# Kernel tuning notes

Measured on AMD Instinct MI355X. Metric: run time of the kernel, lower is better.

The kernel has to match this reference:

```python
import jax, jax.numpy as jnp
import numpy as np

HID = 512
NHEADS = 8
HEAD_DIM = HID // NHEADS  # 64
L = 2048
B = 4
LQ = 128
SCALE = float(np.sqrt(HEAD_DIM))


def _xavier(k, shape):
    lim = float(np.sqrt(6.0 / (shape[0] + shape[1])))
    return jax.random.uniform(k, shape, jnp.float32, -lim, lim)


def setup_inputs() -> dict:
    key = jax.random.key(0)
    ks = jax.random.split(key, 9)
    query = jax.random.normal(ks[0], (L, B, HID), jnp.float32)
    key_t = jax.random.normal(ks[1], (L, B, HID), jnp.float32)
    value = jax.random.normal(ks[2], (L, B, HID), jnp.float32)
    # 1 = pad, 0 = valid (code adds (1-mask).log() to scores)
    key_padding_mask = jax.random.bernoulli(ks[3], 0.1, (B, L)).astype(jnp.float32)
    question_rel_emb = jax.random.normal(ks[4], (LQ, LQ, B, HID), jnp.float32) * 0.02
    Wq = _xavier(ks[5], (HID, HID))
    Wk = _xavier(ks[6], (HID, HID))
    Wv = _xavier(ks[7], (HID, HID))
    Wo = _xavier(ks[8], (HID, HID))
    return dict(query=query, key_t=key_t, value=value,
                key_padding_mask=key_padding_mask,
                question_rel_emb=question_rel_emb,
                Wq=Wq, Wk=Wk, Wv=Wv, Wo=Wo)


def reference(query, key_t, value, key_padding_mask, question_rel_emb, Wq, Wk, Wv, Wo):
    # head_reshape: [L,B,HID] -> [B*K, L, D] (b outer, k inner, matching torch view)
    def heads(x, W):
        y = x @ W.T                                   # [L,B,HID]
        return jnp.swapaxes(y.reshape(L, B * NHEADS, HEAD_DIM), 0, 1)

    q = heads(query, Wq)    # [BK,L,D]
    k = heads(key_t, Wk)
    v = heads(value, Wv)

    attn = jnp.einsum('nld,nmd->nlm', q, k)            # [BK,L,L]

    # question relative bias: proj_key over [Lq,Lq,B,HID] -> [BK,Lq,Lq,D]
    qr = question_rel_emb @ Wk.T
    qr = qr.reshape(LQ, LQ, B * NHEADS, HEAD_DIM).transpose(2, 0, 1, 3)
    bias = jnp.einsum('nijd,nid->nij', qr, q[:, -LQ:])  # [BK,Lq,Lq]
    attn = attn.at[:, -LQ:, -LQ:].add(bias)

    attn = attn / SCALE

    # padding mask: repeat_interleave over batch, add log(1-mask) per key column
    kpm = jnp.repeat(key_padding_mask, NHEADS, axis=0)  # [BK,L]
    attn = attn + jnp.log1p(-kpm)[:, None, :]

    attn = jax.nn.softmax(attn, axis=-1)
    out = jnp.einsum('nlm,nmd->nld', attn, v)           # [BK,L,D]
    out = jnp.swapaxes(out, 0, 1).reshape(L, B, HID) @ Wo.T
    return (out, attn)
```

## Files before the change

### kernel.cpp

```cpp
#include <hip/hip_runtime.h>
#include <hip/hip_bf16.h>


using short8   = __attribute__((ext_vector_type(8))) short;
using short4v  = __attribute__((ext_vector_type(4))) short;
using ushort4v = __attribute__((ext_vector_type(4))) unsigned short;
using f32x4    = __attribute__((ext_vector_type(4))) float;

#define L_T   2048
#define B_T   4
#define HID_T 512
#define HD_T  64
#define LQ_T  128
#define L0_T  1920

__device__ __forceinline__ float b2f(unsigned short u){
  return __uint_as_float(((unsigned int)u) << 16);
}
__device__ __forceinline__ unsigned short f2b(float f){
  unsigned int u = __float_as_uint(f);
  u += 0x7FFFu + ((u >> 16) & 1u);
  return (unsigned short)(u >> 16);
}
__device__ __forceinline__ f32x4 mfma16(short8 a, short8 b, f32x4 c){
  return __builtin_amdgcn_mfma_f32_16x16x32_bf16(a, b, c, 0, 0, 0);
}
#if __has_builtin(__builtin_amdgcn_mfma_f32_16x16x16bf16_1k)
__device__ __forceinline__ f32x4 mfma16k16(short4v a, short4v b, f32x4 c){
  return __builtin_amdgcn_mfma_f32_16x16x16bf16_1k(a, b, c, 0, 0, 0);
}
#else
__device__ __forceinline__ f32x4 mfma16k16(short4v a, short4v b, f32x4 c){
  f32x4 d;
  asm("v_mfma_f32_16x16x16_bf16 %0, %1, %2, %0"
      : "=v"(d) : "v"(a), "v"(b), "0"(c));
  return d;
}
#endif

__global__ __launch_bounds__(256) void k_splitW(const float* __restrict__ w0,
                                                const float* __restrict__ w1,
                                                const float* __restrict__ w2,
                                                const float* __restrict__ w3,
                                                unsigned short* __restrict__ hi,
                                                unsigned short* __restrict__ lo)
{
  int wid = blockIdx.y;
  const float* src = (wid == 0) ? w0 : (wid == 1) ? w1 : (wid == 2) ? w2 : w3;
  int chunk = blockIdx.x * 256 + threadIdx.x;
  int o = chunk >> 7;
  int hpos = (chunk & 127) * 4;
  f32x4 v = ((const f32x4*)src)[chunk];
  ushort4v h4, l4;
  #pragma unroll
  for (int e = 0; e < 4; e++){
    unsigned short h = f2b(v[e]);
    h4[e] = h;
    l4[e] = f2b(v[e] - b2f(h));
  }
  size_t idx = ((size_t)(wid * 512 + (o >> 4) * 16 + (hpos >> 5))) * 512
             + (((hpos & 31) >> 3) * 16 + (o & 15)) * 8 + (hpos & 7);
  *(ushort4v*)(hi + idx) = h4;
  *(ushort4v*)(lo + idx) = l4;
}

__global__ __launch_bounds__(256) void k_proj3(const float* __restrict__ Xq,
                                               const float* __restrict__ Xk,
                                               const float* __restrict__ Xv,
                                               const unsigned short* __restrict__ WhA,
                                               const unsigned short* __restrict__ WlA,
                                               unsigned short* __restrict__ qhp,
                                               unsigned short* __restrict__ qlp,
                                               unsigned short* __restrict__ khp,
                                               unsigned short* __restrict__ klp,
                                               unsigned short* __restrict__ vpk)
{
  int sel = blockIdx.x >> 10;
  int bx  = blockIdx.x & 1023;
  const float* X = (sel == 0) ? Xq : (sel == 1) ? Xk : Xv;
  const short* WH = (const short*)WhA + (size_t)sel * 262144;
  const short* WL = (const short*)WlA + (size_t)sel * 262144;
  unsigned short* ohi = (sel == 0) ? qhp : khp;
  unsigned short* olo = (sel == 0) ? qlp : klp;

  int wv = threadIdx.x >> 6, lane = threadIdx.x & 63;
  int tid = bx * 4 + wv;
  int mt = tid >> 3, nt = tid & 7;
  int row0 = mt * 16, col0 = nt * 64;
  int lhi = lane >> 4, llo = lane & 15;
  int arow = row0 + llo;
  f32x4 acc[4] = {{0,0,0,0},{0,0,0,0},{0,0,0,0},{0,0,0,0}};
  #pragma unroll 4
  for (int k0 = 0; k0 < 512; k0 += 32){
    const float* ap = X + (size_t)arow * 512 + k0 + lhi * 8;
    f32x4 a01 = *(const f32x4*)ap;
    f32x4 a23 = *(const f32x4*)(ap + 4);
    short8 ah, al;
    #pragma unroll
    for (int e = 0; e < 4; e++){
      unsigned short h0 = f2b(a01[e]);
      ah[e] = (short)h0;  al[e] = (short)f2b(a01[e] - b2f(h0));
      unsigned short h1 = f2b(a23[e]);
      ah[e + 4] = (short)h1;  al[e + 4] = (short)f2b(a23[e] - b2f(h1));
    }
    int kk = k0 >> 5;
    #pragma unroll
    for (int cb = 0; cb < 4; cb++){
      size_t bidx = (size_t)(((col0 >> 4) + cb) * 16 + kk) * 512 + lane * 8;
      short8 bh = *(const short8*)(WH + bidx);
      short8 bl = *(const short8*)(WL + bidx);
      acc[cb] = mfma16(ah, bh, acc[cb]);
      acc[cb] = mfma16(al, bh, acc[cb]);
      acc[cb] = mfma16(ah, bl, acc[cb]);
    }
  }
  #pragma unroll
  for (int cb = 0; cb < 4; cb++){
    #pragma unroll
    for (int r = 0; r < 4; r++){
      int row = row0 + lhi * 4 + r;
      int o   = col0 + cb * 16 + llo;
      int l = row >> 2, bb = row & 3;
      int n = bb * 8 + (o >> 6), d = o & 63;
      float v = acc[cb][r];
      if (sel != 2){
        size_t idx = ((size_t)(n * 128 + (l >> 4)) * 2 + (d >> 5)) * 512
                   + (((d & 31) >> 3) * 16 + (l & 15)) * 8 + (d & 7);
        unsigned short h = f2b(v);
        ohi[idx] = h;
        olo[idx] = f2b(v - b2f(h));
      } else {
        int m = l;
        size_t idx = (((size_t)(n * 128 + (m >> 4)) * 4) + (d >> 4)) * 256
                   + ((m & 15) >> 2) * 64 + (d & 15) * 4 + (m & 3);
        vpk[idx] = f2b(v);
      }
    }
  }
}

__global__ __launch_bounds__(256) void k_tb(const unsigned short* __restrict__ qhp,
                                            const unsigned short* __restrict__ qlp,
                                            const float* __restrict__ Wk,
                                            const float* __restrict__ qrem,
                                            float* __restrict__ bias)
{
  int bb = blockIdx.x & 3, i = blockIdx.x >> 2;
  __shared__ float qv[8][64];
  __shared__ float ts[8][512];
  for (int idx = threadIdx.x; idx < 512; idx += 256){
    int kh = idx >> 6, d = idx & 63;
    int n = bb * 8 + kh;
    int row = L0_T + i;
    size_t qidx = ((size_t)(n * 128 + (row >> 4)) * 2 + (d >> 5)) * 512
                + (((d & 31) >> 3) * 16 + (row & 15)) * 8 + (d & 7);
    qv[kh][d] = b2f(qhp[qidx]) + b2f(qlp[qidx]);
  }
  __syncthreads();
  {
    int kh = threadIdx.x >> 5, h0 = (threadIdx.x & 31) * 16;
    f32x4 a0 = {0,0,0,0}, a1 = {0,0,0,0}, a2 = {0,0,0,0}, a3 = {0,0,0,0};
    for (int d = 0; d < 64; d++){
      float qd = qv[kh][d];
      const float* wr = Wk + (size_t)(kh * 64 + d) * 512 + h0;
      a0 += qd * *(const f32x4*)(wr);
      a1 += qd * *(const f32x4*)(wr + 4);
      a2 += qd * *(const f32x4*)(wr + 8);
      a3 += qd * *(const f32x4*)(wr + 12);
    }
    *(f32x4*)&ts[kh][h0]      = a0;
    *(f32x4*)&ts[kh][h0 + 4]  = a1;
    *(f32x4*)&ts[kh][h0 + 8]  = a2;
    *(f32x4*)&ts[kh][h0 + 12] = a3;
  }
  __syncthreads();
  int wv = threadIdx.x >> 6, lane = threadIdx.x & 63;
  for (int j = wv; j < 128; j += 4){
    const float* qr = qrem + (((size_t)i * LQ_T + j) * B_T + bb) * 512;
    f32x4 v0 = *(const f32x4*)(qr + lane * 4);
    f32x4 v1 = *(const f32x4*)(qr + 256 + lane * 4);
    float pl[8];
    #pragma unroll
    for (int kh = 0; kh < 8; kh++){
      f32x4 t0 = *(const f32x4*)&ts[kh][lane * 4];
      f32x4 t1 = *(const f32x4*)&ts[kh][256 + lane * 4];
      pl[kh] = v0[0]*t0[0] + v0[1]*t0[1] + v0[2]*t0[2] + v0[3]*t0[3]
             + v1[0]*t1[0] + v1[1]*t1[1] + v1[2]*t1[2] + v1[3]*t1[3];
    }
    #pragma unroll
    for (int kh = 0; kh < 8; kh++){
      float s = pl[kh];
      #pragma unroll
      for (int msk = 1; msk < 64; msk <<= 1) s += __shfl_xor(s, msk);
      pl[kh] = s;
    }
    if (lane == 0){
      #pragma unroll
      for (int kh = 0; kh < 8; kh++)
        bias[((size_t)(bb * 8 + kh) * LQ_T + i) * LQ_T + j] = pl[kh];
    }
  }
}

__global__ __launch_bounds__(1024, 4) void k_attn(
    const unsigned short* __restrict__ qhp, const unsigned short* __restrict__ qlp,
    const unsigned short* __restrict__ khp, const unsigned short* __restrict__ klp,
    const float* __restrict__ bias, const float* __restrict__ kpm,
    const unsigned short* __restrict__ vpk,
    float* __restrict__ attnF, float* __restrict__ outbk)
{
  __shared__ __attribute__((aligned(16))) float pf[16 * 1024];
  __shared__ float2 red2[2 * 256];
  const int w = threadIdx.x >> 6, lane = threadIdx.x & 63;
  const int lhi = lane >> 4, llo = lane & 15;

  for (int j = 0; j < 8; ++j){
    const int p = blockIdx.x + (j << 8);
    const int n = p >> 6, rbp = p & 63;
    const int rbA = rbp * 2, rbB = rbA + 1;
    const int row0A = rbA * 16, row0B = rbB * 16, bb = n >> 3;

    const short* QHA = (const short*)qhp + ((size_t)(n * 128 + rbA) * 2) * 512 + lane * 8;
    const short* QLA = (const short*)qlp + ((size_t)(n * 128 + rbA) * 2) * 512 + lane * 8;
    const short* QHB = (const short*)qhp + ((size_t)(n * 128 + rbB) * 2) * 512 + lane * 8;
    const short* QLB = (const short*)qlp + ((size_t)(n * 128 + rbB) * 2) * 512 + lane * 8;
    short8 qhA0 = *(const short8*)(QHA);
    short8 qhA1 = *(const short8*)(QHA + 512);
    short8 qlA0 = *(const short8*)(QLA);
    short8 qlA1 = *(const short8*)(QLA + 512);
    short8 qhB0 = *(const short8*)(QHB);
    short8 qhB1 = *(const short8*)(QHB + 512);
    short8 qlB0 = *(const short8*)(QLB);
    short8 qlB1 = *(const short8*)(QLB + 512);
    const short* KH = (const short*)khp + (size_t)n * 131072 + w * 1024 + lane * 8;
    const short* KL = (const short*)klp + (size_t)n * 131072 + w * 1024 + lane * 8;

    float svA[8][4], svB[8][4];
    #pragma unroll
    for (int t = 0; t < 8; t++){
      short8 kh0v = *(const short8*)(KH + t * 16384);
      short8 kh1v = *(const short8*)(KH + t * 16384 + 512);
      short8 kl0v = *(const short8*)(KL + t * 16384);
      short8 kl1v = *(const short8*)(KL + t * 16384 + 512);
      f32x4 aA = {0.f, 0.f, 0.f, 0.f};
      f32x4 aB = {0.f, 0.f, 0.f, 0.f};
      aA = mfma16(kh0v, qhA0, aA);
      aA = mfma16(kl0v, qhA0, aA);
      aA = mfma16(kh0v, qlA0, aA);
      aA = mfma16(kh1v, qhA1, aA);
      aA = mfma16(kl1v, qhA1, aA);
      aA = mfma16(kh1v, qlA1, aA);
      aB = mfma16(kh0v, qhB0, aB);
      aB = mfma16(kl0v, qhB0, aB);
      aB = mfma16(kh0v, qlB0, aB);
      aB = mfma16(kh1v, qhB1, aB);
      aB = mfma16(kl1v, qhB1, aB);
      aB = mfma16(kh1v, qlB1, aB);
      if (t == 7 && rbp >= 60 && w >= 8){
        int j0 = (w - 8) * 16 + lhi * 4;
        int iA = row0A - L0_T + llo;
        int iB = row0B - L0_T + llo;
        aA += *(const f32x4*)(bias + ((size_t)(n * 128 + iA)) * 128 + j0);
        aB += *(const f32x4*)(bias + ((size_t)(n * 128 + iB)) * 128 + j0);
      }
      f32x4 mkv = *(const f32x4*)(kpm + bb * 2048 + (w + t * 16) * 16 + lhi * 4);
      #pragma unroll
      for (int r = 0; r < 4; r++){
        float mk = (mkv[r] != 0.f) ? -__builtin_inff() : 0.f;
        svA[t][r] = aA[r] * 0.125f + mk;
        svB[t][r] = aB[r] * 0.125f + mk;
      }
    }

    float pmA = svA[0][0], pmB = svB[0][0];
    #pragma unroll
    for (int t = 0; t < 8; t++)
      #pragma unroll
      for (int r = 0; r < 4; r++){
        pmA = fmaxf(pmA, svA[t][r]);
        pmB = fmaxf(pmB, svB[t][r]);
      }
    pmA = fmaxf(pmA, __shfl_xor(pmA, 16));
    pmA = fmaxf(pmA, __shfl_xor(pmA, 32));
    pmB = fmaxf(pmB, __shfl_xor(pmB, 16));
    pmB = fmaxf(pmB, __shfl_xor(pmB, 32));
    float esA = 0.f, esB = 0.f;
    #pragma unroll
    for (int t = 0; t < 8; t++)
      #pragma unroll
      for (int r = 0; r < 4; r++){
        float eA = __expf(svA[t][r] - pmA);
        float eB = __expf(svB[t][r] - pmB);
        svA[t][r] = eA;  esA += eA;
        svB[t][r] = eB;  esB += eB;
      }
    esA += __shfl_xor(esA, 16);
    esA += __shfl_xor(esA, 32);
    esB += __shfl_xor(esB, 16);
    esB += __shfl_xor(esB, 32);
    if (lane < 16){
      red2[w * 16 + llo]       = make_float2(pmA, esA);
      red2[256 + w * 16 + llo] = make_float2(pmB, esB);
    }
    asm volatile("s_waitcnt lgkmcnt(0)\n\ts_barrier" ::: "memory");

    float facA, facB;
    {
      float2 c0 = red2[(lhi * 4 + 0) * 16 + llo];
      float2 c1 = red2[(lhi * 4 + 1) * 16 + llo];
      float2 c2 = red2[(lhi * 4 + 2) * 16 + llo];
      float2 c3 = red2[(lhi * 4 + 3) * 16 + llo];
      float mg = fmaxf(fmaxf(c0.x, c1.x), fmaxf(c2.x, c3.x));
      mg = fmaxf(mg, __shfl_xor(mg, 16));
      mg = fmaxf(mg, __shfl_xor(mg, 32));
      float cg = c0.y * __expf(c0.x - mg) + c1.y * __expf(c1.x - mg)
               + c2.y * __expf(c2.x - mg) + c3.y * __expf(c3.x - mg);
      cg += __shfl_xor(cg, 16);
      cg += __shfl_xor(cg, 32);
      facA = __expf(pmA - mg) / cg;
    }
    {
      float2 c0 = red2[256 + (lhi * 4 + 0) * 16 + llo];
      float2 c1 = red2[256 + (lhi * 4 + 1) * 16 + llo];
      float2 c2 = red2[256 + (lhi * 4 + 2) * 16 + llo];
      float2 c3 = red2[256 + (lhi * 4 + 3) * 16 + llo];
      float mg = fmaxf(fmaxf(c0.x, c1.x), fmaxf(c2.x, c3.x));
      mg = fmaxf(mg, __shfl_xor(mg, 16));
      mg = fmaxf(mg, __shfl_xor(mg, 32));
      float cg = c0.y * __expf(c0.x - mg) + c1.y * __expf(c1.x - mg)
               + c2.y * __expf(c2.x - mg) + c3.y * __expf(c3.x - mg);
      cg += __shfl_xor(cg, 16);
      cg += __shfl_xor(cg, 32);
      facB = __expf(pmB - mg) / cg;
    }

    float* aRowA = attnF + ((size_t)(n * L_T + row0A + llo)) * L_T;
    float* aRowB = attnF + ((size_t)(n * L_T + row0B + llo)) * L_T;
    const short* VP = (const short*)vpk + (size_t)n * 131072 + w * 1024 + lane * 4;
    f32x4 pA0 = {0,0,0,0}, pA1 = {0,0,0,0}, pA2 = {0,0,0,0}, pA3 = {0,0,0,0};
    f32x4 pB0 = {0,0,0,0}, pB1 = {0,0,0,0}, pB2 = {0,0,0,0}, pB3 = {0,0,0,0};
    #pragma unroll
    for (int t = 0; t < 8; t++){
      short4v v0 = *(const short4v*)(VP + t * 16384 +   0);
      short4v v1 = *(const short4v*)(VP + t * 16384 + 256);
      short4v v2 = *(const short4v*)(VP + t * 16384 + 512);
      short4v v3 = *(const short4v*)(VP + t * 16384 + 768);
      f32x4 pvA, pvB;
      #pragma unroll
      for (int r = 0; r < 4; r++){
        pvA[r] = svA[t][r] * facA;
        pvB[r] = svB[t][r] * facB;
      }
      __builtin_nontemporal_store(pvA, (f32x4*)(aRowA + (w + t * 16) * 16 + lhi * 4));
      __builtin_nontemporal_store(pvB, (f32x4*)(aRowB + (w + t * 16) * 16 + lhi * 4));
      short4v pbA, pbB;
      #pragma unroll
      for (int r = 0; r < 4; r++){
        pbA[r] = (short)f2b(pvA[r]);
        pbB[r] = (short)f2b(pvB[r]);
      }
      pA0 = mfma16k16(v0, pbA, pA0);
      pA1 = mfma16k16(v1, pbA, pA1);
      pA2 = mfma16k16(v2, pbA, pA2);
      pA3 = mfma16k16(v3, pbA, pA3);
      pB0 = mfma16k16(v0, pbB, pB0);
      pB1 = mfma16k16(v1, pbB, pB1);
      pB2 = mfma16k16(v2, pbB, pB2);
      pB3 = mfma16k16(v3, pbB, pB3);
    }

    float* pfw = pf + w * 1024 + llo * 64;
    *(f32x4*)(pfw + (( 0 + lhi * 4 + llo * 4) & 63)) = pA0;
    *(f32x4*)(pfw + ((16 + lhi * 4 + llo * 4) & 63)) = pA1;
    *(f32x4*)(pfw + ((32 + lhi * 4 + llo * 4) & 63)) = pA2;
    *(f32x4*)(pfw + ((48 + lhi * 4 + llo * 4) & 63)) = pA3;
    asm volatile("s_waitcnt lgkmcnt(0)\n\ts_barrier" ::: "memory");
    {
      int q = w, d = lane;
      int slot = (d + q * 4) & 63;
      float s = 0.f;
      #pragma unroll
      for (int ww = 0; ww < 16; ww++) s += pf[ww * 1024 + q * 64 + slot];
      outbk[((size_t)(n * L_T + row0A + q)) * HD_T + d] = s;
    }
    asm volatile("s_waitcnt lgkmcnt(0)\n\ts_barrier" ::: "memory");
    *(f32x4*)(pfw + (( 0 + lhi * 4 + llo * 4) & 63)) = pB0;
    *(f32x4*)(pfw + ((16 + lhi * 4 + llo * 4) & 63)) = pB1;
    *(f32x4*)(pfw + ((32 + lhi * 4 + llo * 4) & 63)) = pB2;
    *(f32x4*)(pfw + ((48 + lhi * 4 + llo * 4) & 63)) = pB3;
    asm volatile("s_waitcnt lgkmcnt(0)\n\ts_barrier" ::: "memory");
    {
      int q = w, d = lane;
      int slot = (d + q * 4) & 63;
      float s = 0.f;
      #pragma unroll
      for (int ww = 0; ww < 16; ww++) s += pf[ww * 1024 + q * 64 + slot];
      outbk[((size_t)(n * L_T + row0B + q)) * HD_T + d] = s;
    }
  }
}

__global__ __launch_bounds__(256) void k_final(const float* __restrict__ outbk,
                                               const unsigned short* __restrict__ Wh,
                                               const unsigned short* __restrict__ Wl,
                                               float* __restrict__ y)
{
  int wv = threadIdx.x >> 6, lane = threadIdx.x & 63;
  int tid = blockIdx.x * 4 + wv;
  int mt = tid >> 5, nt = tid & 31;
  int row0 = mt * 16, col0 = nt * 16;
  int lhi = lane >> 4, llo = lane & 15;
  int arow = row0 + llo;
  int l = arow >> 2, bb = arow & 3;
  const short* WHs = (const short*)Wh;
  const short* WLs = (const short*)Wl;
  f32x4 acc = {0.f, 0.f, 0.f, 0.f};
  for (int k0 = 0; k0 < 512; k0 += 32){
    int c = k0 + lhi * 8;
    const float* ap = outbk + ((size_t)(bb * 8 + (c >> 6)) * L_T + l) * HD_T + (c & 63);
    f32x4 a01 = *(const f32x4*)ap;
    f32x4 a23 = *(const f32x4*)(ap + 4);
    short8 ahi, alo;
    #pragma unroll
    for (int e = 0; e < 4; e++){
      unsigned short h0 = f2b(a01[e]);
      ahi[e] = (short)h0;  alo[e] = (short)f2b(a01[e] - b2f(h0));
      unsigned short h1 = f2b(a23[e]);
      ahi[e + 4] = (short)h1;  alo[e + 4] = (short)f2b(a23[e] - b2f(h1));
    }
    size_t bidx = (size_t)(nt * 16 + (k0 >> 5)) * 512 + lane * 8;
    short8 bh = *(const short8*)(WHs + bidx);
    short8 bl = *(const short8*)(WLs + bidx);
    acc = mfma16(ahi, bh, acc);
    acc = mfma16(alo, bh, acc);
    acc = mfma16(ahi, bl, acc);
  }
  #pragma unroll
  for (int r = 0; r < 4; r++)
    y[(size_t)(row0 + lhi * 4 + r) * 512 + col0 + llo] = acc[r];
}

extern "C" void kernel_launch(void* const* d_in, const int* in_sizes, int n_in,
                              void* d_out, int out_size, void* d_ws, size_t ws_size,
                              hipStream_t stream)
{
  const float* query = (const float*)d_in[0];
  const float* key_t = (const float*)d_in[1];
  const float* value = (const float*)d_in[2];
  const float* kpm   = (const float*)d_in[3];
  const float* qrem  = (const float*)d_in[4];
  const float* Wq    = (const float*)d_in[5];
  const float* Wk    = (const float*)d_in[6];
  const float* Wv    = (const float*)d_in[7];
  const float* Wo    = (const float*)d_in[8];

  float* outY  = (float*)d_out;
  float* attnF = outY + (size_t)L_T * B_T * HID_T;

  char* wp = (char*)d_ws;
  const size_t SZ8M = (size_t)32 * 2048 * 64 * 2;
  unsigned short* qhp = (unsigned short*)wp; wp += SZ8M;
  unsigned short* qlp = (unsigned short*)wp; wp += SZ8M;
  unsigned short* khp = (unsigned short*)wp; wp += SZ8M;
  unsigned short* klp = (unsigned short*)wp; wp += SZ8M;
  unsigned short* vpk = (unsigned short*)wp; wp += SZ8M;
  unsigned short* whA = (unsigned short*)wp; wp += (size_t)4 * 512 * 512 * 2;
  unsigned short* wlA = (unsigned short*)wp; wp += (size_t)4 * 512 * 512 * 2;
  float* biasb = (float*)wp; wp += (size_t)32 * 128 * 128 * 4;
  float* outbk = (float*)wp; wp += (size_t)32 * 2048 * 64 * 4;

  const size_t WSTEP = (size_t)512 * 512;

  k_splitW<<<dim3(256, 4), 256, 0, stream>>>(Wq, Wk, Wv, Wo, whA, wlA);
  k_proj3<<<3072, 256, 0, stream>>>(query, key_t, value, whA, wlA,
                                    qhp, qlp, khp, klp, vpk);
  k_tb<<<512, 256, 0, stream>>>(qhp, qlp, Wk, qrem, biasb);
  k_attn<<<256, 1024, 0, stream>>>(qhp, qlp, khp, klp, biasb, kpm,
                                   vpk, attnF, outbk);
  k_final<<<4096, 256, 0, stream>>>(outbk, whA + 3 * WSTEP, wlA + 3 * WSTEP, outY);
}
```

Measured before the change: 518.0 us.

## Halve attention block to 8 waves, each covering 16 key tiles

Shrinks k_attn blocks from 16 to 8 waves, so each wave now processes 16 key column tiles instead of 8. The cross-wave softmax reduction and the PV partial-sum reduction are reworked to match, with each wave now reducing two output rows. This cuts shared memory and cross-wave reduction work, and the waves_per_eu attribute gives the compiler more registers per wave. The cost is fewer waves per CU to hide memory latency and double the per-wave score register arrays, which could spill.

After: 470.0 us (median of 2 runs). -9.3%, faster.

```diff
diff --git a/kernel.cpp b/kernel.cpp
--- a/kernel.cpp
+++ b/kernel.cpp
@@ -202,15 +202,16 @@
   }
 }
 
-__global__ __launch_bounds__(1024, 4) void k_attn(
+__attribute__((amdgpu_waves_per_eu(2, 2)))
+__global__ __launch_bounds__(512) void k_attn(
     const unsigned short* __restrict__ qhp, const unsigned short* __restrict__ qlp,
     const unsigned short* __restrict__ khp, const unsigned short* __restrict__ klp,
     const float* __restrict__ bias, const float* __restrict__ kpm,
     const unsigned short* __restrict__ vpk,
     float* __restrict__ attnF, float* __restrict__ outbk)
 {
-  __shared__ __attribute__((aligned(16))) float pf[16 * 1024];
-  __shared__ float2 red2[2 * 256];
+  __shared__ __attribute__((aligned(16))) float pf[8 * 1024];
+  __shared__ float2 red2[2 * 128];
   const int w = threadIdx.x >> 6, lane = threadIdx.x & 63;
   const int lhi = lane >> 4, llo = lane & 15;
 
@@ -235,13 +236,13 @@
     const short* KH = (const short*)khp + (size_t)n * 131072 + w * 1024 + lane * 8;
     const short* KL = (const short*)klp + (size_t)n * 131072 + w * 1024 + lane * 8;
 
-    float svA[8][4], svB[8][4];
-    #pragma unroll
-    for (int t = 0; t < 8; t++){
-      short8 kh0v = *(const short8*)(KH + t * 16384);
-      short8 kh1v = *(const short8*)(KH + t * 16384 + 512);
-      short8 kl0v = *(const short8*)(KL + t * 16384);
-      short8 kl1v = *(const short8*)(KL + t * 16384 + 512);
+    float svA[16][4], svB[16][4];
+    #pragma unroll
+    for (int t = 0; t < 16; t++){
+      short8 kh0v = *(const short8*)(KH + t * 8192);
+      short8 kh1v = *(const short8*)(KH + t * 8192 + 512);
+      short8 kl0v = *(const short8*)(KL + t * 8192);
+      short8 kl1v = *(const short8*)(KL + t * 8192 + 512);
       f32x4 aA = {0.f, 0.f, 0.f, 0.f};
       f32x4 aB = {0.f, 0.f, 0.f, 0.f};
       aA = mfma16(kh0v, qhA0, aA);
@@ -256,14 +257,14 @@
       aB = mfma16(kh1v, qhB1, aB);
       aB = mfma16(kl1v, qhB1, aB);
       aB = mfma16(kh1v, qlB1, aB);
-      if (t == 7 && rbp >= 60 && w >= 8){
-        int j0 = (w - 8) * 16 + lhi * 4;
+      if (t == 15 && rbp >= 60){
+        int j0 = w * 16 + lhi * 4;
         int iA = row0A - L0_T + llo;
         int iB = row0B - L0_T + llo;
         aA += *(const f32x4*)(bias + ((size_t)(n * 128 + iA)) * 128 + j0);
         aB += *(const f32x4*)(bias + ((size_t)(n * 128 + iB)) * 128 + j0);
       }
-      f32x4 mkv = *(const f32x4*)(kpm + bb * 2048 + (w + t * 16) * 16 + lhi * 4);
+      f32x4 mkv = *(const f32x4*)(kpm + bb * 2048 + (w + t * 8) * 16 + lhi * 4);
       #pragma unroll
       for (int r = 0; r < 4; r++){
         float mk = (mkv[r] != 0.f) ? -__builtin_inff() : 0.f;
@@ -274,7 +275,7 @@
 
     float pmA = svA[0][0], pmB = svB[0][0];
     #pragma unroll
-    for (int t = 0; t < 8; t++)
+    for (int t = 0; t < 16; t++)
       #pragma unroll
       for (int r = 0; r < 4; r++){
         pmA = fmaxf(pmA, svA[t][r]);
@@ -286,7 +287,7 @@
     pmB = fmaxf(pmB, __shfl_xor(pmB, 32));
     float esA = 0.f, esB = 0.f;
     #pragma unroll
-    for (int t = 0; t < 8; t++)
+    for (int t = 0; t < 16; t++)
       #pragma unroll
       for (int r = 0; r < 4; r++){
         float eA = __expf(svA[t][r] - pmA);
@@ -300,35 +301,29 @@
     esB += __shfl_xor(esB, 32);
     if (lane < 16){
       red2[w * 16 + llo]       = make_float2(pmA, esA);
-      red2[256 + w * 16 + llo] = make_float2(pmB, esB);
+      red2[128 + w * 16 + llo] = make_float2(pmB, esB);
     }
     asm volatile("s_waitcnt lgkmcnt(0)\n\ts_barrier" ::: "memory");
 
     float facA, facB;
     {
-      float2 c0 = red2[(lhi * 4 + 0) * 16 + llo];
-      float2 c1 = red2[(lhi * 4 + 1) * 16 + llo];
-      float2 c2 = red2[(lhi * 4 + 2) * 16 + llo];
-      float2 c3 = red2[(lhi * 4 + 3) * 16 + llo];
-      float mg = fmaxf(fmaxf(c0.x, c1.x), fmaxf(c2.x, c3.x));
+      float2 c0 = red2[(lhi * 2 + 0) * 16 + llo];
+      float2 c1 = red2[(lhi * 2 + 1) * 16 + llo];
+      float mg = fmaxf(c0.x, c1.x);
       mg = fmaxf(mg, __shfl_xor(mg, 16));
       mg = fmaxf(mg, __shfl_xor(mg, 32));
-      float cg = c0.y * __expf(c0.x - mg) + c1.y * __expf(c1.x - mg)
-               + c2.y * __expf(c2.x - mg) + c3.y * __expf(c3.x - mg);
+      float cg = c0.y * __expf(c0.x - mg) + c1.y * __expf(c1.x - mg);
       cg += __shfl_xor(cg, 16);
       cg += __shfl_xor(cg, 32);
       facA = __expf(pmA - mg) / cg;
     }
     {
-      float2 c0 = red2[256 + (lhi * 4 + 0) * 16 + llo];
-      float2 c1 = red2[256 + (lhi * 4 + 1) * 16 + llo];
-      float2 c2 = red2[256 + (lhi * 4 + 2) * 16 + llo];
-      float2 c3 = red2[256 + (lhi * 4 + 3) * 16 + llo];
-      float mg = fmaxf(fmaxf(c0.x, c1.x), fmaxf(c2.x, c3.x));
+      float2 c0 = red2[128 + (lhi * 2 + 0) * 16 + llo];
+      float2 c1 = red2[128 + (lhi * 2 + 1) * 16 + llo];
+      float mg = fmaxf(c0.x, c1.x);
       mg = fmaxf(mg, __shfl_xor(mg, 16));
       mg = fmaxf(mg, __shfl_xor(mg, 32));
-      float cg = c0.y * __expf(c0.x - mg) + c1.y * __expf(c1.x - mg)
-               + c2.y * __expf(c2.x - mg) + c3.y * __expf(c3.x - mg);
+      float cg = c0.y * __expf(c0.x - mg) + c1.y * __expf(c1.x - mg);
       cg += __shfl_xor(cg, 16);
       cg += __shfl_xor(cg, 32);
       facB = __expf(pmB - mg) / cg;
@@ -340,19 +335,19 @@
     f32x4 pA0 = {0,0,0,0}, pA1 = {0,0,0,0}, pA2 = {0,0,0,0}, pA3 = {0,0,0,0};
     f32x4 pB0 = {0,0,0,0}, pB1 = {0,0,0,0}, pB2 = {0,0,0,0}, pB3 = {0,0,0,0};
     #pragma unroll
-    for (int t = 0; t < 8; t++){
-      short4v v0 = *(const short4v*)(VP + t * 16384 +   0);
-      short4v v1 = *(const short4v*)(VP + t * 16384 + 256);
-      short4v v2 = *(const short4v*)(VP + t * 16384 + 512);
-      short4v v3 = *(const short4v*)(VP + t * 16384 + 768);
+    for (int t = 0; t < 16; t++){
+      short4v v0 = *(const short4v*)(VP + t * 8192 +   0);
+      short4v v1 = *(const short4v*)(VP + t * 8192 + 256);
+      short4v v2 = *(const short4v*)(VP + t * 8192 + 512);
+      short4v v3 = *(const short4v*)(VP + t * 8192 + 768);
       f32x4 pvA, pvB;
       #pragma unroll
       for (int r = 0; r < 4; r++){
         pvA[r] = svA[t][r] * facA;
         pvB[r] = svB[t][r] * facB;
       }
-      __builtin_nontemporal_store(pvA, (f32x4*)(aRowA + (w + t * 16) * 16 + lhi * 4));
-      __builtin_nontemporal_store(pvB, (f32x4*)(aRowB + (w + t * 16) * 16 + lhi * 4));
+      __builtin_nontemporal_store(pvA, (f32x4*)(aRowA + (w + t * 8) * 16 + lhi * 4));
+      __builtin_nontemporal_store(pvB, (f32x4*)(aRowB + (w + t * 8) * 16 + lhi * 4));
       short4v pbA, pbB;
       #pragma unroll
       for (int r = 0; r < 4; r++){
@@ -376,12 +371,19 @@
     *(f32x4*)(pfw + ((48 + lhi * 4 + llo * 4) & 63)) = pA3;
     asm volatile("s_waitcnt lgkmcnt(0)\n\ts_barrier" ::: "memory");
     {
-      int q = w, d = lane;
+      int d = lane;
+      int q = w;
       int slot = (d + q * 4) & 63;
       float s = 0.f;
       #pragma unroll
-      for (int ww = 0; ww < 16; ww++) s += pf[ww * 1024 + q * 64 + slot];
+      for (int ww = 0; ww < 8; ww++) s += pf[ww * 1024 + q * 64 + slot];
       outbk[((size_t)(n * L_T + row0A + q)) * HD_T + d] = s;
+      int q2 = w + 8;
+      int slot2 = (d + q2 * 4) & 63;
+      float s2 = 0.f;
+      #pragma unroll
+      for (int ww = 0; ww < 8; ww++) s2 += pf[ww * 1024 + q2 * 64 + slot2];
+      outbk[((size_t)(n * L_T + row0A + q2)) * HD_T + d] = s2;
     }
     asm volatile("s_waitcnt lgkmcnt(0)\n\ts_barrier" ::: "memory");
     *(f32x4*)(pfw + (( 0 + lhi * 4 + llo * 4) & 63)) = pB0;
@@ -390,12 +392,19 @@
     *(f32x4*)(pfw + ((48 + lhi * 4 + llo * 4) & 63)) = pB3;
     asm volatile("s_waitcnt lgkmcnt(0)\n\ts_barrier" ::: "memory");
     {
-      int q = w, d = lane;
+      int d = lane;
+      int q = w;
       int slot = (d + q * 4) & 63;
       float s = 0.f;
       #pragma unroll
-      for (int ww = 0; ww < 16; ww++) s += pf[ww * 1024 + q * 64 + slot];
+      for (int ww = 0; ww < 8; ww++) s += pf[ww * 1024 + q * 64 + slot];
       outbk[((size_t)(n * L_T + row0B + q)) * HD_T + d] = s;
+      int q2 = w + 8;
+      int slot2 = (d + q2 * 4) & 63;
+      float s2 = 0.f;
+      #pragma unroll
+      for (int ww = 0; ww < 8; ww++) s2 += pf[ww * 1024 + q2 * 64 + slot2];
+      outbk[((size_t)(n * L_T + row0B + q2)) * HD_T + d] = s2;
     }
   }
 }
@@ -475,7 +484,7 @@
   k_proj3<<<3072, 256, 0, stream>>>(query, key_t, value, whA, wlA,
                                     qhp, qlp, khp, klp, vpk);
   k_tb<<<512, 256, 0, stream>>>(qhp, qlp, Wk, qrem, biasb);
-  k_attn<<<256, 1024, 0, stream>>>(qhp, qlp, khp, klp, biasb, kpm,
-                                   vpk, attnF, outbk);
+  k_attn<<<256, 512, 0, stream>>>(qhp, qlp, khp, klp, biasb, kpm,
+                                  vpk, attnF, outbk);
   k_final<<<4096, 256, 0, stream>>>(outbk, whA + 3 * WSTEP, wlA + 3 * WSTEP, outY);
 }
```
